# Performance work log

Hardware: AMD Instinct MI355X
Metric: run time of the kernel (lower is better)

## Reference

```python
import jax, jax.numpy as jnp
import numpy as np

B, S, E, NH = 2, 2048, 1024, 4
HD = E // NH  # 256


def setup_inputs() -> dict:
    key = jax.random.key(0)
    ks = jax.random.split(key, 8)
    return {
        "q": jax.random.normal(ks[0], (B, S, E), jnp.float32),
        "k": jax.random.normal(ks[1], (B, S, E), jnp.float32),
        "v": jax.random.normal(ks[2], (B, S, E), jnp.float32),
        # gate Dense params (kernel zero-init in the module; use small random for a nontrivial baseline)
        "igate_kernel": jax.random.normal(ks[3], (3 * E, NH), jnp.float32) * 0.02,
        "igate_bias": jax.random.normal(ks[4], (NH,), jnp.float32) * 0.1,
        "fgate_kernel": jax.random.normal(ks[5], (3 * E, NH), jnp.float32) * 0.02,
        "fgate_bias": jnp.linspace(3.0, 6.0, NH, dtype=jnp.float32),  # bias_linspace_init
        "rms_scale": jax.random.normal(ks[6], (HD,), jnp.float32) * 0.02,
    }


def _mlstm_head(q, k, v, ig, fg, eps=1e-06):
    # q,k,v: (S, DH); ig, fg: (S, 1)
    s, dh = q.shape
    log_f = jax.nn.log_sigmoid(fg)                       # (S,1)
    cs = jnp.concatenate([jnp.zeros((1, 1), log_f.dtype),
                          jnp.cumsum(log_f, axis=0)], axis=0)  # (S+1,1)
    neg = jnp.asarray(-0.7 * jnp.finfo(cs.dtype).max, cs.dtype)
    log_d = jnp.where(jnp.tri(s, dtype=bool),
                      (cs - cs.T)[1:, 1:] + ig.T, neg)   # (S,S)
    m = jnp.max(log_d, axis=-1, keepdims=True)           # row-wise stabilizer
    d = jnp.exp(log_d - m)
    c = (q @ (k.T / jnp.sqrt(dh))) * d                   # (S,S)
    n = jnp.maximum(jnp.sum(c, axis=-1, keepdims=True), jnp.exp(-m))
    return (c / (n + eps)) @ v                           # (S,DH)


def reference(q, k, v, igate_kernel, igate_bias, fgate_kernel, fgate_bias, rms_scale):
    b, s, e = q.shape
    nh = igate_kernel.shape[1]
    hd = e // nh
    gate_in = jnp.concatenate((q, k, v), axis=-1)                 # (B,S,3E)
    ig = (gate_in @ igate_kernel + igate_bias).swapaxes(-1, -2)[..., None]  # (B,NH,S,1)
    fg = (gate_in @ fgate_kernel + fgate_bias).swapaxes(-1, -2)[..., None]  # (B,NH,S,1)
    qh = q.reshape(b, s, nh, hd).swapaxes(1, 2)                   # (B,NH,S,HD)
    kh = k.reshape(b, s, nh, hd).swapaxes(1, 2)
    vh = v.reshape(b, s, nh, hd).swapaxes(1, 2)
    h = jax.vmap(jax.vmap(_mlstm_head))(qh, kh, vh, ig, fg)      # (B,NH,S,HD)
    # RMSNorm over head_dim with (1+scale)
    var = jnp.mean(jnp.square(h.astype(jnp.float32)), axis=-1, keepdims=True)
    h = (h * jax.lax.rsqrt(var + 1e-06)).astype(h.dtype) * (1.0 + rms_scale)
    return h.swapaxes(1, 2).reshape(b, s, e)
```

## Files before the change

kernel.cpp:

```cpp
#include <hip/hip_runtime.h>
#include <math.h>

static constexpr int B_  = 2;
static constexpr int S_  = 2048;
static constexpr int E_  = 1024;
static constexpr int NH_ = 4;
static constexpr int HD_ = 256;
static constexpr int BH_ = B_ * NH_;

typedef __attribute__((ext_vector_type(8))) _Float16 half8;
typedef __attribute__((ext_vector_type(4))) float    f32x4;
typedef __attribute__((ext_vector_type(4))) _Float16 half4v;

__global__ __launch_bounds__(1024) void prep_kernel(
    const float* __restrict__ q, const float* __restrict__ k, const float* __restrict__ v,
    const float* __restrict__ igk, const float* __restrict__ igb,
    const float* __restrict__ fgk, const float* __restrict__ fgb,
    float* __restrict__ ig_out, float* __restrict__ fg_out,
    _Float16* __restrict__ Qh, _Float16* __restrict__ Kh, _Float16* __restrict__ Vt)
{
    __shared__ __align__(16) char PSM[98304];
    float4* wi = (float4*)PSM;
    float4* wf = wi + 3 * E_;

    const int t = threadIdx.x;
    #pragma unroll
    for (int i = 0; i < 3; ++i) {
        int e = t + 1024 * i;
        wi[e] = ((const float4*)igk)[e];
        wf[e] = ((const float4*)fgk)[e];
    }
    __syncthreads();

    const int wave = t >> 6;
    const int l    = t & 63;
    const int bs   = blockIdx.x * 16 + wave;
    const int b = bs >> 11, s = bs & (S_ - 1);
    const float* qrow = q + (size_t)bs * E_;
    const float* krow = k + (size_t)bs * E_;
    const float* vrow = v + (size_t)bs * E_;

    float accI[4] = {0.f,0.f,0.f,0.f}, accF[4] = {0.f,0.f,0.f,0.f};
    #pragma unroll
    for (int j = 0; j < 48; ++j) {
        const int e = l + 64 * j;
        float g;
        if (j < 16)       g = qrow[e];
        else if (j < 32)  g = krow[e - E_];
        else              g = vrow[e - 2 * E_];
        if (j < 16) {
            int hh = e >> 8, d = e & 255;
            Qh[(((size_t)(b * NH_ + hh)) * S_ + s) * HD_ + d] = (_Float16)(g * 0.0625f);
        } else if (j < 32) {
            int e2 = e - E_; int hh = e2 >> 8, d = e2 & 255;
            Kh[(((size_t)(b * NH_ + hh)) * S_ + s) * HD_ + d] = (_Float16)g;
        }
        float4 wiv = wi[e];
        float4 wfv = wf[e];
        accI[0] = fmaf(g, wiv.x, accI[0]); accI[1] = fmaf(g, wiv.y, accI[1]);
        accI[2] = fmaf(g, wiv.z, accI[2]); accI[3] = fmaf(g, wiv.w, accI[3]);
        accF[0] = fmaf(g, wfv.x, accF[0]); accF[1] = fmaf(g, wfv.y, accF[1]);
        accF[2] = fmaf(g, wfv.z, accF[2]); accF[3] = fmaf(g, wfv.w, accF[3]);
    }
    #pragma unroll
    for (int m = 1; m < 64; m <<= 1) {
        #pragma unroll
        for (int h = 0; h < 4; ++h) {
            accI[h] += __shfl_xor(accI[h], m);
            accF[h] += __shfl_xor(accF[h], m);
        }
    }
    if (l == 0) {
        #pragma unroll
        for (int h = 0; h < 4; ++h) {
            ig_out[((size_t)(b * NH_ + h)) * S_ + s] = accI[h] + igb[h];
            fg_out[((size_t)(b * NH_ + h)) * S_ + s] = accF[h] + fgb[h];
        }
    }

    __syncthreads();
    {
        float (*tile)[65] = (float(*)[65])(PSM + (t >> 8) * 16640);
        const int tid = t & 255;
        const int m  = blockIdx.x * 4 + (t >> 8);
        const int bh = m & 7;
        const int sb = (m >> 3) & 31;
        const int db = m >> 8;
        const int bb = bh >> 2, hh = bh & 3;
        const int j4 = (tid & 15) * 4;
        const int i0 = tid >> 4;
        const float* src = v + ((size_t)(bb * S_ + sb * 64)) * E_ + hh * HD_ + db * 64;
        #pragma unroll
        for (int p = 0; p < 4; ++p) {
            int i = i0 + p * 16;
            float4 val = *(const float4*)(src + (size_t)i * E_ + j4);
            tile[i][j4] = val.x; tile[i][j4+1] = val.y; tile[i][j4+2] = val.z; tile[i][j4+3] = val.w;
        }
        __syncthreads();
        const int s4 = (tid & 15) * 4;
        const int d0 = tid >> 4;
        _Float16* dst = Vt + ((size_t)bh * HD_ + db * 64) * S_ + sb * 64;
        #pragma unroll
        for (int p = 0; p < 4; ++p) {
            int d = d0 + p * 16;
            half4v pk;
            pk.x = (_Float16)tile[s4][d];   pk.y = (_Float16)tile[s4+1][d];
            pk.z = (_Float16)tile[s4+2][d]; pk.w = (_Float16)tile[s4+3][d];
            *(half4v*)(dst + (size_t)d * S_ + s4) = pk;
        }
    }
}

static constexpr int PB_BYTES = 32 * 128 * 2;
static constexpr int OFF_AMM = 2 * PB_BYTES;
static constexpr int OFF_G   = OFF_AMM + S_ * 4;
static constexpr int OFF_M   = OFF_G + S_ * 4;
static constexpr int OFF_RS  = OFF_M + S_ * 4;
static constexpr int OFF_SS  = OFF_RS + 8 * 32 * 4;
static constexpr int OFF_WR  = OFF_SS + 8 * 32 * 4;
static constexpr int SMB     = OFF_WR + 64;

__global__ __launch_bounds__(512, 2) void mlstm_kernel(
    const _Float16* __restrict__ Qh, const _Float16* __restrict__ Kh,
    const _Float16* __restrict__ Vt,
    const float* __restrict__ ig, const float* __restrict__ fg,
    const float* __restrict__ rms_scale, float* __restrict__ out)
{
    __shared__ __align__(16) char SMEM[SMB];
    char*  Pb    = SMEM;
    float* sAmM  = (float*)(SMEM + OFF_AMM);
    float* sG    = (float*)(SMEM + OFF_G);
    float* sM    = (float*)(SMEM + OFF_M);
    float* rsumP = (float*)(SMEM + OFF_RS);
    float* ssP   = (float*)(SMEM + OFF_SS);
    float* wred  = (float*)(SMEM + OFF_WR);
    float* wred2 = wred + 8;

    const int z  = blockIdx.x;
    const int bh = z & 7;
    const int u  = z >> 3;
    const int b  = bh >> 2, h = bh & 3;
    const int t  = threadIdx.x;
    const int w  = t >> 6;
    const int l  = t & 63;
    const int col  = l & 15;
    const int quad = l >> 4;
    const int qo   = quad * 8;

    {
        const float* fgp = fg + (size_t)bh * S_;
        const float* igp = ig + (size_t)bh * S_;
        float4 fx = *(const float4*)(fgp + t * 4);
        float4 ix = *(const float4*)(igp + t * 4);
        float xi[4] = {fx.x, fx.y, fx.z, fx.w};
        float gi[4] = {ix.x, ix.y, ix.z, ix.w};
        float ls[4];
        float run = 0.f;
        #pragma unroll
        for (int i = 0; i < 4; ++i) {
            float x = xi[i];
            float lg = (x >= 0.f) ? -log1pf(expf(-x)) : (x - log1pf(expf(x)));
            run += lg;
            ls[i] = run;
        }
        const float own = run;
        #pragma unroll
        for (int m = 1; m < 64; m <<= 1) {
            float o = __shfl_up(run, m);
            if (l >= m) run += o;
        }
        if (l == 63) wred[w] = run;
        __syncthreads();
        float wpre = 0.f;
        for (int ww = 0; ww < w; ++ww) wpre += wred[ww];
        const float exclT = wpre + run - own;
        float A[4], g[4], gm[4];
        float rmax = -__builtin_inff();
        #pragma unroll
        for (int i = 0; i < 4; ++i) {
            A[i] = exclT + ls[i];
            g[i] = gi[i] - A[i];
            rmax = fmaxf(rmax, g[i]);
            gm[i] = rmax;
        }
        float sm = rmax;
        #pragma unroll
        for (int m = 1; m < 64; m <<= 1) {
            float o = __shfl_up(sm, m);
            if (l >= m) sm = fmaxf(sm, o);
        }
        if (l == 63) wred2[w] = sm;
        __syncthreads();
        float exm = -__builtin_inff();
        for (int ww = 0; ww < w; ++ww) exm = fmaxf(exm, wred2[ww]);
        float up = __shfl_up(sm, 1);
        if (l > 0) exm = fmaxf(exm, up);
        #pragma unroll
        for (int i = 0; i < 4; ++i) {
            float cm = fmaxf(exm, gm[i]);
            float Mi = A[i] + cm;
            sAmM[t * 4 + i] = A[i] - Mi;
            sG[t * 4 + i]   = g[i];
            sM[t * 4 + i]   = Mi;
        }
        __syncthreads();
    }

    const _Float16* Qp  = Qh + (size_t)bh * S_ * HD_;
    const _Float16* Kp  = Kh + (size_t)bh * S_ * HD_;
    const _Float16* Vtp = Vt + (size_t)bh * HD_ * S_;

    const float rsc0 = 1.f + rms_scale[w * 32 + col];
    const float rsc1 = 1.f + rms_scale[w * 32 + 16 + col];

    int buf = 0;

    for (int pass = 0; pass < 2; ++pass) {
        const int rb = pass ? (63 - u) : u;
        const int rowbase = rb * 32;
        const int Tt = (rb >> 2) + 1;

        half8 qf0[8], qf1[8];
        #pragma unroll
        for (int kk = 0; kk < 8; ++kk) {
            qf0[kk] = *(const half8*)(Qp + (size_t)(rowbase + col) * HD_ + kk * 32 + qo);
            qf1[kk] = *(const half8*)(Qp + (size_t)(rowbase + 16 + col) * HD_ + kk * 32 + qo);
        }
        float amM0[4], amM1[4];
        #pragma unroll
        for (int rr = 0; rr < 4; ++rr) {
            amM0[rr] = sAmM[rowbase + quad * 4 + rr];
            amM1[rr] = sAmM[rowbase + 16 + quad * 4 + rr];
        }

        f32x4 acc[4];
        #pragma unroll
        for (int i = 0; i < 4; ++i) acc[i] = (f32x4){0.f, 0.f, 0.f, 0.f};
        float rs0[4] = {0.f,0.f,0.f,0.f}, rs1[4] = {0.f,0.f,0.f,0.f};

        const _Float16* kcol_base = Kp + (size_t)(w * 16 + col) * HD_ + qo;
        half8 kf[8];
        #pragma unroll
        for (int kk = 0; kk < 8; ++kk)
            kf[kk] = *(const half8*)(kcol_base + kk * 32);

        half8 vf[8];
        for (int jt = 0; jt < Tt; ++jt) {
            const int c0 = jt << 7;
            #pragma unroll
            for (int nsub = 0; nsub < 2; ++nsub) {
                #pragma unroll
                for (int kh = 0; kh < 4; ++kh)
                    vf[nsub * 4 + kh] = *(const half8*)(Vtp
                        + (size_t)(w * 32 + nsub * 16 + col) * S_ + c0 + kh * 32 + qo);
            }
            f32x4 sc0 = (f32x4){0.f,0.f,0.f,0.f}, sc1 = (f32x4){0.f,0.f,0.f,0.f};
            #pragma unroll
            for (int kk = 0; kk < 8; ++kk) {
                sc0 = __builtin_amdgcn_mfma_f32_16x16x32_f16(qf0[kk], kf[kk], sc0, 0, 0, 0);
                sc1 = __builtin_amdgcn_mfma_f32_16x16x32_f16(qf1[kk], kf[kk], sc1, 0, 0, 0);
            }
            if (jt + 1 < Tt) {
                const _Float16* kb = kcol_base + (size_t)(c0 + 128) * HD_;
                #pragma unroll
                for (int kk = 0; kk < 8; ++kk)
                    kf[kk] = *(const half8*)(kb + kk * 32);
            }
            const int gcol = c0 + w * 16 + col;
            const float gv = sG[gcol];
            char* pbC = Pb + buf * PB_BYTES;
            const int hcb = (w * 16 + col) << 1;
            #pragma unroll
            for (int rr = 0; rr < 4; ++rr) {
                const int r0 = quad * 4 + rr;
                const int sw = (r0 & 7) << 4;
                float e0 = __expf(amM0[rr] + gv);
                float p0 = (gcol <= rowbase + r0) ? sc0[rr] * e0 : 0.f;
                rs0[rr] += p0;
                *(_Float16*)(pbC + (((r0 << 8) + hcb) ^ sw)) = (_Float16)p0;
                float e1 = __expf(amM1[rr] + gv);
                float p1 = (gcol <= rowbase + 16 + r0) ? sc1[rr] * e1 : 0.f;
                rs1[rr] += p1;
                const int r1 = r0 + 16;
                *(_Float16*)(pbC + (((r1 << 8) + hcb) ^ sw)) = (_Float16)p1;
            }
            __syncthreads();
            #pragma unroll
            for (int rsub = 0; rsub < 2; ++rsub) {
                const int prow = rsub * 16 + col;
                half8 af[4];
                #pragma unroll
                for (int kh = 0; kh < 4; ++kh)
                    af[kh] = *(const half8*)(pbC
                        + ((prow << 8) + ((kh * 64 + qo * 2) ^ ((col & 7) << 4))));
                #pragma unroll
                for (int kh = 0; kh < 4; ++kh) {
                    acc[rsub * 2 + 0] = __builtin_amdgcn_mfma_f32_16x16x32_f16(af[kh], vf[kh],     acc[rsub * 2 + 0], 0, 0, 0);
                    acc[rsub * 2 + 1] = __builtin_amdgcn_mfma_f32_16x16x32_f16(af[kh], vf[4 + kh], acc[rsub * 2 + 1], 0, 0, 0);
                }
            }
            buf ^= 1;
        }

        #pragma unroll
        for (int m = 1; m < 16; m <<= 1) {
            #pragma unroll
            for (int rr = 0; rr < 4; ++rr) {
                rs0[rr] += __shfl_xor(rs0[rr], m);
                rs1[rr] += __shfl_xor(rs1[rr], m);
            }
        }
        if (col == 0) {
            #pragma unroll
            for (int rr = 0; rr < 4; ++rr) {
                rsumP[w * 32 + quad * 4 + rr]      = rs0[rr];
                rsumP[w * 32 + 16 + quad * 4 + rr] = rs1[rr];
            }
        }
        __syncthreads();
        float inv0[4], inv1[4];
        #pragma unroll
        for (int rr = 0; rr < 4; ++rr) {
            const int r0 = quad * 4 + rr;
            float tot0 = 0.f, tot1 = 0.f;
            #pragma unroll
            for (int ww = 0; ww < 8; ++ww) {
                tot0 += rsumP[ww * 32 + r0];
                tot1 += rsumP[ww * 32 + 16 + r0];
            }
            float M0 = sM[rowbase + r0];
            float M1 = sM[rowbase + 16 + r0];
            inv0[rr] = 1.0f / (fmaxf(tot0, __expf(-M0)) + 1e-6f);
            inv1[rr] = 1.0f / (fmaxf(tot1, __expf(-M1)) + 1e-6f);
        }
        float ss0[4] = {0.f,0.f,0.f,0.f}, ss1[4] = {0.f,0.f,0.f,0.f};
        #pragma unroll
        for (int nsub = 0; nsub < 2; ++nsub) {
            #pragma unroll
            for (int rr = 0; rr < 4; ++rr) {
                float h0 = acc[nsub][rr] * inv0[rr];
                acc[nsub][rr] = h0;
                ss0[rr] = fmaf(h0, h0, ss0[rr]);
                float h1 = acc[2 + nsub][rr] * inv1[rr];
                acc[2 + nsub][rr] = h1;
                ss1[rr] = fmaf(h1, h1, ss1[rr]);
            }
        }
        #pragma unroll
        for (int m = 1; m < 16; m <<= 1) {
            #pragma unroll
            for (int rr = 0; rr < 4; ++rr) {
                ss0[rr] += __shfl_xor(ss0[rr], m);
                ss1[rr] += __shfl_xor(ss1[rr], m);
            }
        }
        if (col == 0) {
            #pragma unroll
            for (int rr = 0; rr < 4; ++rr) {
                ssP[w * 32 + quad * 4 + rr]      = ss0[rr];
                ssP[w * 32 + 16 + quad * 4 + rr] = ss1[rr];
            }
        }
        __syncthreads();
        #pragma unroll
        for (int rr = 0; rr < 4; ++rr) {
            const int r0 = quad * 4 + rr;
            float sst0 = 0.f, sst1 = 0.f;
            #pragma unroll
            for (int ww = 0; ww < 8; ++ww) {
                sst0 += ssP[ww * 32 + r0];
                sst1 += ssP[ww * 32 + 16 + r0];
            }
            float rstd0 = rsqrtf(sst0 * (1.0f / HD_) + 1e-6f);
            float rstd1 = rsqrtf(sst1 * (1.0f / HD_) + 1e-6f);
            float* o0 = out + ((size_t)(b * S_ + rowbase + r0)) * E_ + h * HD_ + w * 32;
            float* o1 = out + ((size_t)(b * S_ + rowbase + 16 + r0)) * E_ + h * HD_ + w * 32;
            o0[col]      = acc[0][rr] * rstd0 * rsc0;
            o0[16 + col] = acc[1][rr] * rstd0 * rsc1;
            o1[col]      = acc[2][rr] * rstd1 * rsc0;
            o1[16 + col] = acc[3][rr] * rstd1 * rsc1;
        }
        __syncthreads();
    }
}

extern "C" void kernel_launch(void* const* d_in, const int* in_sizes, int n_in,
                              void* d_out, int out_size, void* d_ws, size_t ws_size,
                              hipStream_t stream) {
    (void)in_sizes; (void)n_in; (void)out_size; (void)ws_size;
    const float* q   = (const float*)d_in[0];
    const float* k   = (const float*)d_in[1];
    const float* v   = (const float*)d_in[2];
    const float* igk = (const float*)d_in[3];
    const float* igb = (const float*)d_in[4];
    const float* fgk = (const float*)d_in[5];
    const float* fgb = (const float*)d_in[6];
    const float* rsc = (const float*)d_in[7];
    float* out = (float*)d_out;

    float* ws  = (float*)d_ws;
    float* ig  = ws;
    float* fg  = ws + (size_t)BH_ * S_;
    _Float16* Qh = (_Float16*)(ws + (size_t)2 * BH_ * S_);
    _Float16* Kh = Qh + (size_t)BH_ * S_ * HD_;
    _Float16* Vt = Kh + (size_t)BH_ * S_ * HD_;

    prep_kernel<<<B_ * S_ / 16, 1024, 0, stream>>>(q, k, v, igk, igb, fgk, fgb,
                                                   ig, fg, Qh, Kh, Vt);
    mlstm_kernel<<<BH_ * 32, 512, 0, stream>>>(Qh, Kh, Vt, ig, fg, rsc, out);
}
```

Baseline: 184.6 us.

## Split mLSTM passes into separate blocks, vectorize prep loads, raise occupancy

```diff
diff --git a/kernel.cpp b/kernel.cpp
--- a/kernel.cpp
+++ b/kernel.cpp
@@ -42,25 +42,36 @@
 
     float accI[4] = {0.f,0.f,0.f,0.f}, accF[4] = {0.f,0.f,0.f,0.f};
     #pragma unroll
-    for (int j = 0; j < 48; ++j) {
-        const int e = l + 64 * j;
-        float g;
-        if (j < 16)       g = qrow[e];
-        else if (j < 32)  g = krow[e - E_];
-        else              g = vrow[e - 2 * E_];
-        if (j < 16) {
-            int hh = e >> 8, d = e & 255;
-            Qh[(((size_t)(b * NH_ + hh)) * S_ + s) * HD_ + d] = (_Float16)(g * 0.0625f);
-        } else if (j < 32) {
-            int e2 = e - E_; int hh = e2 >> 8, d = e2 & 255;
-            Kh[(((size_t)(b * NH_ + hh)) * S_ + s) * HD_ + d] = (_Float16)g;
-        }
-        float4 wiv = wi[e];
-        float4 wfv = wf[e];
-        accI[0] = fmaf(g, wiv.x, accI[0]); accI[1] = fmaf(g, wiv.y, accI[1]);
-        accI[2] = fmaf(g, wiv.z, accI[2]); accI[3] = fmaf(g, wiv.w, accI[3]);
-        accF[0] = fmaf(g, wfv.x, accF[0]); accF[1] = fmaf(g, wfv.y, accF[1]);
-        accF[2] = fmaf(g, wfv.z, accF[2]); accF[3] = fmaf(g, wfv.w, accF[3]);
+    for (int j = 0; j < 12; ++j) {
+        const int e4 = l * 4 + 256 * j;
+        float4 g4;
+        if (j < 4)       g4 = *(const float4*)(qrow + e4);
+        else if (j < 8)  g4 = *(const float4*)(krow + (e4 - E_));
+        else             g4 = *(const float4*)(vrow + (e4 - 2 * E_));
+        const float ge[4] = {g4.x, g4.y, g4.z, g4.w};
+        if (j < 4) {
+            const int d = e4 & 255, hh = e4 >> 8;
+            half4v st;
+            st.x = (_Float16)(ge[0] * 0.0625f); st.y = (_Float16)(ge[1] * 0.0625f);
+            st.z = (_Float16)(ge[2] * 0.0625f); st.w = (_Float16)(ge[3] * 0.0625f);
+            *(half4v*)(Qh + (((size_t)(b * NH_ + hh)) * S_ + s) * HD_ + d) = st;
+        } else if (j < 8) {
+            const int e2 = e4 - E_;
+            const int d = e2 & 255, hh = e2 >> 8;
+            half4v st;
+            st.x = (_Float16)ge[0]; st.y = (_Float16)ge[1];
+            st.z = (_Float16)ge[2]; st.w = (_Float16)ge[3];
+            *(half4v*)(Kh + (((size_t)(b * NH_ + hh)) * S_ + s) * HD_ + d) = st;
+        }
+        #pragma unroll
+        for (int i = 0; i < 4; ++i) {
+            float4 wiv = wi[e4 + i];
+            float4 wfv = wf[e4 + i];
+            accI[0] = fmaf(ge[i], wiv.x, accI[0]); accI[1] = fmaf(ge[i], wiv.y, accI[1]);
+            accI[2] = fmaf(ge[i], wiv.z, accI[2]); accI[3] = fmaf(ge[i], wiv.w, accI[3]);
+            accF[0] = fmaf(ge[i], wfv.x, accF[0]); accF[1] = fmaf(ge[i], wfv.y, accF[1]);
+            accF[2] = fmaf(ge[i], wfv.z, accF[2]); accF[3] = fmaf(ge[i], wfv.w, accF[3]);
+        }
     }
     #pragma unroll
     for (int m = 1; m < 64; m <<= 1) {
@@ -120,7 +131,7 @@
 static constexpr int OFF_WR  = OFF_SS + 8 * 32 * 4;
 static constexpr int SMB     = OFF_WR + 64;
 
-__global__ __launch_bounds__(512, 2) void mlstm_kernel(
+__global__ __launch_bounds__(512, 4) void mlstm_kernel(
     const _Float16* __restrict__ Qh, const _Float16* __restrict__ Kh,
     const _Float16* __restrict__ Vt,
     const float* __restrict__ ig, const float* __restrict__ fg,
@@ -138,7 +149,8 @@
 
     const int z  = blockIdx.x;
     const int bh = z & 7;
-    const int u  = z >> 3;
+    const int u  = (z >> 3) & 31;
+    const int pass = z >> 8;
     const int b  = bh >> 2, h = bh & 3;
     const int t  = threadIdx.x;
     const int w  = t >> 6;
@@ -215,172 +227,170 @@
 
     int buf = 0;
 
-    for (int pass = 0; pass < 2; ++pass) {
-        const int rb = pass ? (63 - u) : u;
-        const int rowbase = rb * 32;
-        const int Tt = (rb >> 2) + 1;
-
-        half8 qf0[8], qf1[8];
-        #pragma unroll
-        for (int kk = 0; kk < 8; ++kk) {
-            qf0[kk] = *(const half8*)(Qp + (size_t)(rowbase + col) * HD_ + kk * 32 + qo);
-            qf1[kk] = *(const half8*)(Qp + (size_t)(rowbase + 16 + col) * HD_ + kk * 32 + qo);
-        }
-        float amM0[4], amM1[4];
-        #pragma unroll
-        for (int rr = 0; rr < 4; ++rr) {
-            amM0[rr] = sAmM[rowbase + quad * 4 + rr];
-            amM1[rr] = sAmM[rowbase + 16 + quad * 4 + rr];
-        }
-
-        f32x4 acc[4];
-        #pragma unroll
-        for (int i = 0; i < 4; ++i) acc[i] = (f32x4){0.f, 0.f, 0.f, 0.f};
-        float rs0[4] = {0.f,0.f,0.f,0.f}, rs1[4] = {0.f,0.f,0.f,0.f};
-
-        const _Float16* kcol_base = Kp + (size_t)(w * 16 + col) * HD_ + qo;
-        half8 kf[8];
-        #pragma unroll
-        for (int kk = 0; kk < 8; ++kk)
-            kf[kk] = *(const half8*)(kcol_base + kk * 32);
-
-        half8 vf[8];
-        for (int jt = 0; jt < Tt; ++jt) {
-            const int c0 = jt << 7;
-            #pragma unroll
-            for (int nsub = 0; nsub < 2; ++nsub) {
-                #pragma unroll
-                for (int kh = 0; kh < 4; ++kh)
-                    vf[nsub * 4 + kh] = *(const half8*)(Vtp
-                        + (size_t)(w * 32 + nsub * 16 + col) * S_ + c0 + kh * 32 + qo);
-            }
-            f32x4 sc0 = (f32x4){0.f,0.f,0.f,0.f}, sc1 = (f32x4){0.f,0.f,0.f,0.f};
-            #pragma unroll
-            for (int kk = 0; kk < 8; ++kk) {
-                sc0 = __builtin_amdgcn_mfma_f32_16x16x32_f16(qf0[kk], kf[kk], sc0, 0, 0, 0);
-                sc1 = __builtin_amdgcn_mfma_f32_16x16x32_f16(qf1[kk], kf[kk], sc1, 0, 0, 0);
-            }
-            if (jt + 1 < Tt) {
-                const _Float16* kb = kcol_base + (size_t)(c0 + 128) * HD_;
-                #pragma unroll
-                for (int kk = 0; kk < 8; ++kk)
-                    kf[kk] = *(const half8*)(kb + kk * 32);
-            }
-            const int gcol = c0 + w * 16 + col;
-            const float gv = sG[gcol];
-            char* pbC = Pb + buf * PB_BYTES;
-            const int hcb = (w * 16 + col) << 1;
-            #pragma unroll
-            for (int rr = 0; rr < 4; ++rr) {
-                const int r0 = quad * 4 + rr;
-                const int sw = (r0 & 7) << 4;
-                float e0 = __expf(amM0[rr] + gv);
-                float p0 = (gcol <= rowbase + r0) ? sc0[rr] * e0 : 0.f;
-                rs0[rr] += p0;
-                *(_Float16*)(pbC + (((r0 << 8) + hcb) ^ sw)) = (_Float16)p0;
-                float e1 = __expf(amM1[rr] + gv);
-                float p1 = (gcol <= rowbase + 16 + r0) ? sc1[rr] * e1 : 0.f;
-                rs1[rr] += p1;
-                const int r1 = r0 + 16;
-                *(_Float16*)(pbC + (((r1 << 8) + hcb) ^ sw)) = (_Float16)p1;
-            }
-            __syncthreads();
-            #pragma unroll
-            for (int rsub = 0; rsub < 2; ++rsub) {
-                const int prow = rsub * 16 + col;
-                half8 af[4];
-                #pragma unroll
-                for (int kh = 0; kh < 4; ++kh)
-                    af[kh] = *(const half8*)(pbC
-                        + ((prow << 8) + ((kh * 64 + qo * 2) ^ ((col & 7) << 4))));
-                #pragma unroll
-                for (int kh = 0; kh < 4; ++kh) {
-                    acc[rsub * 2 + 0] = __builtin_amdgcn_mfma_f32_16x16x32_f16(af[kh], vf[kh],     acc[rsub * 2 + 0], 0, 0, 0);
-                    acc[rsub * 2 + 1] = __builtin_amdgcn_mfma_f32_16x16x32_f16(af[kh], vf[4 + kh], acc[rsub * 2 + 1], 0, 0, 0);
-                }
-            }
-            buf ^= 1;
-        }
-
-        #pragma unroll
-        for (int m = 1; m < 16; m <<= 1) {
-            #pragma unroll
-            for (int rr = 0; rr < 4; ++rr) {
-                rs0[rr] += __shfl_xor(rs0[rr], m);
-                rs1[rr] += __shfl_xor(rs1[rr], m);
-            }
-        }
-        if (col == 0) {
-            #pragma unroll
-            for (int rr = 0; rr < 4; ++rr) {
-                rsumP[w * 32 + quad * 4 + rr]      = rs0[rr];
-                rsumP[w * 32 + 16 + quad * 4 + rr] = rs1[rr];
-            }
-        }
-        __syncthreads();
-        float inv0[4], inv1[4];
-        #pragma unroll
-        for (int rr = 0; rr < 4; ++rr) {
-            const int r0 = quad * 4 + rr;
-            float tot0 = 0.f, tot1 = 0.f;
-            #pragma unroll
-            for (int ww = 0; ww < 8; ++ww) {
-                tot0 += rsumP[ww * 32 + r0];
-                tot1 += rsumP[ww * 32 + 16 + r0];
-            }
-            float M0 = sM[rowbase + r0];
-            float M1 = sM[rowbase + 16 + r0];
-            inv0[rr] = 1.0f / (fmaxf(tot0, __expf(-M0)) + 1e-6f);
-            inv1[rr] = 1.0f / (fmaxf(tot1, __expf(-M1)) + 1e-6f);
-        }
-        float ss0[4] = {0.f,0.f,0.f,0.f}, ss1[4] = {0.f,0.f,0.f,0.f};
+    const int rb = pass ? (63 - u) : u;
+    const int rowbase = rb * 32;
+    const int Tt = (rb >> 2) + 1;
+
+    half8 qf0[8], qf1[8];
+    #pragma unroll
+    for (int kk = 0; kk < 8; ++kk) {
+        qf0[kk] = *(const half8*)(Qp + (size_t)(rowbase + col) * HD_ + kk * 32 + qo);
+        qf1[kk] = *(const half8*)(Qp + (size_t)(rowbase + 16 + col) * HD_ + kk * 32 + qo);
+    }
+    float amM0[4], amM1[4];
+    #pragma unroll
+    for (int rr = 0; rr < 4; ++rr) {
+        amM0[rr] = sAmM[rowbase + quad * 4 + rr];
+        amM1[rr] = sAmM[rowbase + 16 + quad * 4 + rr];
+    }
+
+    f32x4 acc[4];
+    #pragma unroll
+    for (int i = 0; i < 4; ++i) acc[i] = (f32x4){0.f, 0.f, 0.f, 0.f};
+    float rs0[4] = {0.f,0.f,0.f,0.f}, rs1[4] = {0.f,0.f,0.f,0.f};
+
+    const _Float16* kcol_base = Kp + (size_t)(w * 16 + col) * HD_ + qo;
+    half8 kf[8];
+    #pragma unroll
+    for (int kk = 0; kk < 8; ++kk)
+        kf[kk] = *(const half8*)(kcol_base + kk * 32);
+
+    half8 vf[8];
+    for (int jt = 0; jt < Tt; ++jt) {
+        const int c0 = jt << 7;
         #pragma unroll
         for (int nsub = 0; nsub < 2; ++nsub) {
             #pragma unroll
-            for (int rr = 0; rr < 4; ++rr) {
-                float h0 = acc[nsub][rr] * inv0[rr];
-                acc[nsub][rr] = h0;
-                ss0[rr] = fmaf(h0, h0, ss0[rr]);
-                float h1 = acc[2 + nsub][rr] * inv1[rr];
-                acc[2 + nsub][rr] = h1;
-                ss1[rr] = fmaf(h1, h1, ss1[rr]);
+            for (int kh = 0; kh < 4; ++kh)
+                vf[nsub * 4 + kh] = *(const half8*)(Vtp
+                    + (size_t)(w * 32 + nsub * 16 + col) * S_ + c0 + kh * 32 + qo);
+        }
+        f32x4 sc0 = (f32x4){0.f,0.f,0.f,0.f}, sc1 = (f32x4){0.f,0.f,0.f,0.f};
+        #pragma unroll
+        for (int kk = 0; kk < 8; ++kk) {
+            sc0 = __builtin_amdgcn_mfma_f32_16x16x32_f16(qf0[kk], kf[kk], sc0, 0, 0, 0);
+            sc1 = __builtin_amdgcn_mfma_f32_16x16x32_f16(qf1[kk], kf[kk], sc1, 0, 0, 0);
+        }
+        if (jt + 1 < Tt) {
+            const _Float16* kb = kcol_base + (size_t)(c0 + 128) * HD_;
+            #pragma unroll
+            for (int kk = 0; kk < 8; ++kk)
+                kf[kk] = *(const half8*)(kb + kk * 32);
+        }
+        const int gcol = c0 + w * 16 + col;
+        const float gv = sG[gcol];
+        char* pbC = Pb + buf * PB_BYTES;
+        const int hcb = (w * 16 + col) << 1;
+        #pragma unroll
+        for (int rr = 0; rr < 4; ++rr) {
+            const int r0 = quad * 4 + rr;
+            const int sw = (r0 & 7) << 4;
+            float e0 = __expf(amM0[rr] + gv);
+            float p0 = (gcol <= rowbase + r0) ? sc0[rr] * e0 : 0.f;
+            rs0[rr] += p0;
+            *(_Float16*)(pbC + (((r0 << 8) + hcb) ^ sw)) = (_Float16)p0;
+            float e1 = __expf(amM1[rr] + gv);
+            float p1 = (gcol <= rowbase + 16 + r0) ? sc1[rr] * e1 : 0.f;
+            rs1[rr] += p1;
+            const int r1 = r0 + 16;
+            *(_Float16*)(pbC + (((r1 << 8) + hcb) ^ sw)) = (_Float16)p1;
+        }
+        asm volatile("s_waitcnt lgkmcnt(0)" ::: "memory");
+        __builtin_amdgcn_s_barrier();
+        #pragma unroll
+        for (int rsub = 0; rsub < 2; ++rsub) {
+            const int prow = rsub * 16 + col;
+            half8 af[4];
+            #pragma unroll
+            for (int kh = 0; kh < 4; ++kh)
+                af[kh] = *(const half8*)(pbC
+                    + ((prow << 8) + ((kh * 64 + qo * 2) ^ ((col & 7) << 4))));
+            #pragma unroll
+            for (int kh = 0; kh < 4; ++kh) {
+                acc[rsub * 2 + 0] = __builtin_amdgcn_mfma_f32_16x16x32_f16(af[kh], vf[kh],     acc[rsub * 2 + 0], 0, 0, 0);
+                acc[rsub * 2 + 1] = __builtin_amdgcn_mfma_f32_16x16x32_f16(af[kh], vf[4 + kh], acc[rsub * 2 + 1], 0, 0, 0);
             }
         }
-        #pragma unroll
-        for (int m = 1; m < 16; m <<= 1) {
-            #pragma unroll
-            for (int rr = 0; rr < 4; ++rr) {
-                ss0[rr] += __shfl_xor(ss0[rr], m);
-                ss1[rr] += __shfl_xor(ss1[rr], m);
-            }
-        }
-        if (col == 0) {
-            #pragma unroll
-            for (int rr = 0; rr < 4; ++rr) {
-                ssP[w * 32 + quad * 4 + rr]      = ss0[rr];
-                ssP[w * 32 + 16 + quad * 4 + rr] = ss1[rr];
-            }
-        }
-        __syncthreads();
-        #pragma unroll
-        for (int rr = 0; rr < 4; ++rr) {
-            const int r0 = quad * 4 + rr;
-            float sst0 = 0.f, sst1 = 0.f;
-            #pragma unroll
-            for (int ww = 0; ww < 8; ++ww) {
-                sst0 += ssP[ww * 32 + r0];
-                sst1 += ssP[ww * 32 + 16 + r0];
-            }
-            float rstd0 = rsqrtf(sst0 * (1.0f / HD_) + 1e-6f);
-            float rstd1 = rsqrtf(sst1 * (1.0f / HD_) + 1e-6f);
-            float* o0 = out + ((size_t)(b * S_ + rowbase + r0)) * E_ + h * HD_ + w * 32;
-            float* o1 = out + ((size_t)(b * S_ + rowbase + 16 + r0)) * E_ + h * HD_ + w * 32;
-            o0[col]      = acc[0][rr] * rstd0 * rsc0;
-            o0[16 + col] = acc[1][rr] * rstd0 * rsc1;
-            o1[col]      = acc[2][rr] * rstd1 * rsc0;
-            o1[16 + col] = acc[3][rr] * rstd1 * rsc1;
-        }
-        __syncthreads();
+        buf ^= 1;
+    }
+
+    #pragma unroll
+    for (int m = 1; m < 16; m <<= 1) {
+        #pragma unroll
+        for (int rr = 0; rr < 4; ++rr) {
+            rs0[rr] += __shfl_xor(rs0[rr], m);
+            rs1[rr] += __shfl_xor(rs1[rr], m);
+        }
+    }
+    if (col == 0) {
+        #pragma unroll
+        for (int rr = 0; rr < 4; ++rr) {
+            rsumP[w * 32 + quad * 4 + rr]      = rs0[rr];
+            rsumP[w * 32 + 16 + quad * 4 + rr] = rs1[rr];
+        }
+    }
+    __syncthreads();
+    float inv0[4], inv1[4];
+    #pragma unroll
+    for (int rr = 0; rr < 4; ++rr) {
+        const int r0 = quad * 4 + rr;
+        float tot0 = 0.f, tot1 = 0.f;
+        #pragma unroll
+        for (int ww = 0; ww < 8; ++ww) {
+            tot0 += rsumP[ww * 32 + r0];
+            tot1 += rsumP[ww * 32 + 16 + r0];
+        }
+        float M0 = sM[rowbase + r0];
+        float M1 = sM[rowbase + 16 + r0];
+        inv0[rr] = 1.0f / (fmaxf(tot0, __expf(-M0)) + 1e-6f);
+        inv1[rr] = 1.0f / (fmaxf(tot1, __expf(-M1)) + 1e-6f);
+    }
+    float ss0[4] = {0.f,0.f,0.f,0.f}, ss1[4] = {0.f,0.f,0.f,0.f};
+    #pragma unroll
+    for (int nsub = 0; nsub < 2; ++nsub) {
+        #pragma unroll
+        for (int rr = 0; rr < 4; ++rr) {
+            float h0 = acc[nsub][rr] * inv0[rr];
+            acc[nsub][rr] = h0;
+            ss0[rr] = fmaf(h0, h0, ss0[rr]);
+            float h1 = acc[2 + nsub][rr] * inv1[rr];
+            acc[2 + nsub][rr] = h1;
+            ss1[rr] = fmaf(h1, h1, ss1[rr]);
+        }
+    }
+    #pragma unroll
+    for (int m = 1; m < 16; m <<= 1) {
+        #pragma unroll
+        for (int rr = 0; rr < 4; ++rr) {
+            ss0[rr] += __shfl_xor(ss0[rr], m);
+            ss1[rr] += __shfl_xor(ss1[rr], m);
+        }
+    }
+    if (col == 0) {
+        #pragma unroll
+        for (int rr = 0; rr < 4; ++rr) {
+            ssP[w * 32 + quad * 4 + rr]      = ss0[rr];
+            ssP[w * 32 + 16 + quad * 4 + rr] = ss1[rr];
+        }
+    }
+    __syncthreads();
+    #pragma unroll
+    for (int rr = 0; rr < 4; ++rr) {
+        const int r0 = quad * 4 + rr;
+        float sst0 = 0.f, sst1 = 0.f;
+        #pragma unroll
+        for (int ww = 0; ww < 8; ++ww) {
+            sst0 += ssP[ww * 32 + r0];
+            sst1 += ssP[ww * 32 + 16 + r0];
+        }
+        float rstd0 = rsqrtf(sst0 * (1.0f / HD_) + 1e-6f);
+        float rstd1 = rsqrtf(sst1 * (1.0f / HD_) + 1e-6f);
+        float* o0 = out + ((size_t)(b * S_ + rowbase + r0)) * E_ + h * HD_ + w * 32;
+        float* o1 = out + ((size_t)(b * S_ + rowbase + 16 + r0)) * E_ + h * HD_ + w * 32;
+        o0[col]      = acc[0][rr] * rstd0 * rsc0;
+        o0[16 + col] = acc[1][rr] * rstd0 * rsc1;
+        o1[col]      = acc[2][rr] * rstd1 * rsc0;
+        o1[16 + col] = acc[3][rr] * rstd1 * rsc1;
     }
 }
 
@@ -407,5 +417,5 @@
 
     prep_kernel<<<B_ * S_ / 16, 1024, 0, stream>>>(q, k, v, igk, igb, fgk, fgb,
                                                    ig, fg, Qh, Kh, Vt);
-    mlstm_kernel<<<BH_ * 32, 512, 0, stream>>>(Qh, Kh, Vt, ig, fg, rsc, out);
+    mlstm_kernel<<<BH_ * 64, 512, 0, stream>>>(Qh, Kh, Vt, ig, fg, rsc, out);
 }
```

After: 300.3 us. +62.6%, slower.
